# Performance work log

Measured on AMD Instinct MI355X. Metric: run time of the kernel, lower is better.

The kernel has to match this reference:

```python
import jax, jax.numpy as jnp
import numpy as np

D_MODEL = 1024
NUM_HEADS = 16
HEAD_DIM = D_MODEL // NUM_HEADS


def setup_inputs() -> dict:
    key = jax.random.key(0)
    ks = jax.random.split(key, 10)
    B, L = 2, 2048
    s = 1.0 / np.sqrt(D_MODEL)
    x = jax.random.normal(ks[0], (B, L, D_MODEL), dtype=jnp.float32)
    Wq = jax.random.normal(ks[1], (D_MODEL, D_MODEL), dtype=jnp.float32) * s
    bq = jnp.zeros((D_MODEL,), dtype=jnp.float32)
    Wk = jax.random.normal(ks[2], (D_MODEL, D_MODEL), dtype=jnp.float32) * s
    bk = jnp.zeros((D_MODEL,), dtype=jnp.float32)
    Wv = jax.random.normal(ks[3], (D_MODEL, D_MODEL), dtype=jnp.float32) * s
    bv = jnp.zeros((D_MODEL,), dtype=jnp.float32)
    Wo = jax.random.normal(ks[4], (D_MODEL, D_MODEL), dtype=jnp.float32) * s
    bo = jnp.zeros((D_MODEL,), dtype=jnp.float32)
    # per-head retention decay; torch init is ones, use values near 1 for nontrivial decay
    gamma = jax.random.uniform(ks[5], (NUM_HEADS,), dtype=jnp.float32, minval=0.95, maxval=1.0)
    return {"x": x, "Wq": Wq, "bq": bq, "Wk": Wk, "bk": bk,
            "Wv": Wv, "bv": bv, "Wo": Wo, "bo": bo, "gamma": gamma}


def reference(x, Wq, bq, Wk, bk, Wv, bv, Wo, bo, gamma):
    B, L, D = x.shape
    H, hd = NUM_HEADS, HEAD_DIM
    # projections (torch Linear: x @ W.T + b), split heads -> [B, H, L, hd]
    q = (x @ Wq.T + bq).reshape(B, L, H, hd).transpose(0, 2, 1, 3)
    k = (x @ Wk.T + bk).reshape(B, L, H, hd).transpose(0, 2, 1, 3)
    v = (x @ Wv.T + bv).reshape(B, L, H, hd).transpose(0, 2, 1, 3)
    # per-head decay gamma_h^i applied along the query index (matches torch broadcast)
    idx = jnp.arange(L, dtype=x.dtype)
    decay = gamma[None, :, None, None] ** idx[None, None, :, None]  # [1, H, L, 1]
    scores = jnp.einsum('bhqd,bhkd->bhqk', q, k)  # [B, H, L, L]
    causal = jnp.tril(jnp.ones((L, L), dtype=x.dtype))
    scores = scores * causal[None, None] * decay
    out = jnp.einsum('bhqk,bhkd->bhqd', scores, v)  # [B, H, L, hd]
    out = out.transpose(0, 2, 1, 3).reshape(B, L, D)
    return out @ Wo.T + bo
```

## Files before the change

### kernel.cpp

```cpp
#include <hip/hip_runtime.h>
#include <hip/hip_bf16.h>

#define D_MODEL 1024
#define NUM_HEADS 16
#define HEAD_DIM 64
#define BATCH 2
#define SEQ 2048
#define M_TOT (BATCH*SEQ)
#define CHUNK 64
#define NCHUNK (SEQ/CHUNK)
#define LT 68

typedef __attribute__((ext_vector_type(8))) short bf16x8;
typedef __attribute__((ext_vector_type(8))) unsigned short us16x8;
typedef __attribute__((ext_vector_type(4))) float f32x4;

__device__ inline ushort f2bf(float f) {
    __hip_bfloat16 h = __float2bfloat16(f);
    return __builtin_bit_cast(ushort, h);
}
__device__ inline float bf2f(ushort u) {
    unsigned int v = ((unsigned int)u) << 16;
    return __builtin_bit_cast(float, v);
}

__device__ inline bf16x8 ld_frag(const ushort* p) {
    struct S { uint2 a, b; };
    S s;
    s.a = *(const uint2*)p;
    s.b = *(const uint2*)(p + 4);
    return __builtin_bit_cast(bf16x8, s);
}

__device__ inline void st16(ushort* dst, uint4 a, uint4 b) {
    *(uint2*)(dst + 0)  = make_uint2(a.x, a.y);
    *(uint2*)(dst + 4)  = make_uint2(a.z, a.w);
    *(uint2*)(dst + 8)  = make_uint2(b.x, b.y);
    *(uint2*)(dst + 12) = make_uint2(b.z, b.w);
}

__device__ inline void load_lds16(const ushort* g, ushort* l) {
    __builtin_amdgcn_global_load_lds(
        (const __attribute__((address_space(1))) unsigned int*)g,
        (__attribute__((address_space(3))) unsigned int*)l, 16, 0, 0);
}

#define XN (M_TOT * D_MODEL)
#define WN (D_MODEL * D_MODEL)
#define CAST_BLOCKS ((XN + 4 * WN) / 4 / 256)
__global__ __launch_bounds__(256) void cast_all_kernel(const float* __restrict__ x,
                                                       const float* __restrict__ Wq,
                                                       const float* __restrict__ Wk,
                                                       const float* __restrict__ Wv,
                                                       const float* __restrict__ Wo,
                                                       ushort* __restrict__ dst,
                                                       const float* __restrict__ gamma,
                                                       float* __restrict__ decay) {
    int bx = blockIdx.x;
    if (bx >= CAST_BLOCKS) {
        int idx = (bx - CAST_BLOCKS) * 256 + threadIdx.x;
        int i = idx >> 4, h = idx & 15;
        decay[idx] = powf(gamma[h], (float)i);
        return;
    }
    size_t o = ((size_t)bx * 256 + threadIdx.x) * 4;
    const float* src;
    if (o < XN)               src = x  + o;
    else if (o < XN + WN)     src = Wq + (o - XN);
    else if (o < XN + 2 * WN) src = Wk + (o - XN - WN);
    else if (o < XN + 3 * WN) src = Wv + (o - XN - 2 * (size_t)WN);
    else                      src = Wo + (o - XN - 3 * (size_t)WN);
    float4 f = *(const float4*)src;
    ushort4 u;
    u.x = f2bf(f.x); u.y = f2bf(f.y); u.z = f2bf(f.z); u.w = f2bf(f.w);
    *(ushort4*)(dst + o) = u;
}

__global__ __launch_bounds__(256, 8) void gemm_qkv(const ushort* __restrict__ A,
                                                   const ushort* __restrict__ Bt,
                                                   const float* __restrict__ b0,
                                                   const float* __restrict__ b1,
                                                   const float* __restrict__ b2,
                                                   ushort* __restrict__ o0,
                                                   ushort* __restrict__ o1,
                                                   ushort* __restrict__ o2,
                                                   const float* __restrict__ decay) {
    const int K = 1024;
    __shared__ ushort lds_a[64 * 64];
    __shared__ ushort lds_b[64 * 64];
    int t = threadIdx.x, lane = t & 63, w = t >> 6;
    int bm = blockIdx.y * 64, bn = blockIdx.x * 64;
    int wm = (w >> 1) * 32, wn = (w & 1) * 32;

    int lr = lane >> 3, lc = lane & 7;
    int gcol = lc ^ (lr & 7);
    const ushort* aBase = A  + (size_t)(bm + w * 16 + lr) * K + gcol * 8;
    const ushort* bBase = Bt + (size_t)(bn + w * 16 + lr) * K + gcol * 8;
    ushort* aLds = &lds_a[(w * 16) * 64];
    ushort* bLds = &lds_b[(w * 16) * 64];

    f32x4 acc[2][2];
    #pragma unroll
    for (int i = 0; i < 2; i++)
        #pragma unroll
        for (int j = 0; j < 2; j++)
            acc[i][j] = (f32x4){0.f, 0.f, 0.f, 0.f};

    int mrel = lane & 15, kq = lane >> 4;

    for (int k0 = 0; k0 < K; k0 += 64) {
        load_lds16(aBase + k0, aLds);
        load_lds16(aBase + (size_t)8 * K + k0, aLds + 512);
        load_lds16(bBase + k0, bLds);
        load_lds16(bBase + (size_t)8 * K + k0, bLds + 512);
        __syncthreads();
        #pragma unroll
        for (int s = 0; s < 2; s++) {
            bf16x8 af[2], bfv[2];
            #pragma unroll
            for (int i = 0; i < 2; i++) {
                int row = wm + i * 16 + mrel;
                af[i] = ld_frag(&lds_a[row * 64 + (((s * 4 + kq) ^ (row & 7)) * 8)]);
            }
            #pragma unroll
            for (int j = 0; j < 2; j++) {
                int row = wn + j * 16 + mrel;
                bfv[j] = ld_frag(&lds_b[row * 64 + (((s * 4 + kq) ^ (row & 7)) * 8)]);
            }
            #pragma unroll
            for (int i = 0; i < 2; i++)
                #pragma unroll
                for (int j = 0; j < 2; j++)
                    acc[i][j] = __builtin_amdgcn_mfma_f32_16x16x32_bf16(af[i], bfv[j], acc[i][j], 0, 0, 0);
        }
        __syncthreads();
    }

    int quad = lane >> 4;
    int buf = bn >> 10;
    const float* bias = (buf == 0) ? b0 : (buf == 1) ? b1 : b2;
    ushort* dstv = (buf == 0) ? o0 : (buf == 1) ? o1 : o2;
    int cbase = (bn & 1023) + wn;
    #pragma unroll
    for (int j = 0; j < 2; j++) {
        int cl = cbase + j * 16 + mrel;
        float bv = bias[cl];
        #pragma unroll
        for (int i = 0; i < 2; i++) {
            #pragma unroll
            for (int reg = 0; reg < 4; reg++) {
                int row = bm + wm + i * 16 + quad * 4 + reg;
                float v = acc[i][j][reg] + bv;
                if (buf == 0)
                    v *= decay[(row & (SEQ - 1)) * 16 + (cl >> 6)];
                dstv[(size_t)row * 1024 + cl] = f2bf(v);
            }
        }
    }
}

__global__ __launch_bounds__(256) void gemm64_wo(const ushort* __restrict__ A,
                                                 const ushort* __restrict__ Bt,
                                                 const float* __restrict__ bias,
                                                 float* __restrict__ C) {
    const int K = 1024;
    __shared__ ushort lds_a[64 * 128];
    __shared__ ushort lds_b[64 * 128];
    int t = threadIdx.x, lane = t & 63, w = t >> 6;
    int bm = blockIdx.y * 64, bn = blockIdx.x * 64;
    int wm = (w >> 1) * 32, wn = (w & 1) * 32;

    int lr4 = lane >> 4;
    int lc16 = lane & 15;
    const ushort* aP[4];
    const ushort* bP[4];
    ushort* aL[4];
    ushort* bL[4];
    #pragma unroll
    for (int s = 0; s < 4; s++) {
        int rowRel = s * 4 + lr4;
        int gc = lc16 ^ (rowRel & 7);
        aP[s] = A  + (size_t)(bm + w * 16 + rowRel) * K + gc * 8;
        bP[s] = Bt + (size_t)(bn + w * 16 + rowRel) * K + gc * 8;
        aL[s] = &lds_a[(w * 16 + s * 4) * 128];
        bL[s] = &lds_b[(w * 16 + s * 4) * 128];
    }

    f32x4 acc[2][2];
    #pragma unroll
    for (int i = 0; i < 2; i++)
        #pragma unroll
        for (int j = 0; j < 2; j++)
            acc[i][j] = (f32x4){0.f, 0.f, 0.f, 0.f};

    int mrel = lane & 15, kq = lane >> 4;

    for (int k0 = 0; k0 < K; k0 += 128) {
        #pragma unroll
        for (int s = 0; s < 4; s++) {
            load_lds16(aP[s] + k0, aL[s]);
            load_lds16(bP[s] + k0, bL[s]);
        }
        __syncthreads();
        #pragma unroll
        for (int s = 0; s < 4; s++) {
            bf16x8 af[2], bfv[2];
            #pragma unroll
            for (int i = 0; i < 2; i++) {
                int row = wm + i * 16 + mrel;
                af[i] = ld_frag(&lds_a[row * 128 + (((s * 4 + kq) ^ (row & 7)) * 8)]);
            }
            #pragma unroll
            for (int j = 0; j < 2; j++) {
                int row = wn + j * 16 + mrel;
                bfv[j] = ld_frag(&lds_b[row * 128 + (((s * 4 + kq) ^ (row & 7)) * 8)]);
            }
            #pragma unroll
            for (int i = 0; i < 2; i++)
                #pragma unroll
                for (int j = 0; j < 2; j++)
                    acc[i][j] = __builtin_amdgcn_mfma_f32_16x16x32_bf16(af[i], bfv[j], acc[i][j], 0, 0, 0);
        }
        __syncthreads();
    }

    int quad = lane >> 4;
    #pragma unroll
    for (int j = 0; j < 2; j++) {
        int col = bn + wn + j * 16 + mrel;
        float bv = bias[col];
        #pragma unroll
        for (int i = 0; i < 2; i++) {
            #pragma unroll
            for (int reg = 0; reg < 4; reg++) {
                int row = bm + wm + i * 16 + quad * 4 + reg;
                C[(size_t)row * 1024 + col] = acc[i][j][reg] + bv;
            }
        }
    }
}

__global__ __launch_bounds__(256) void chunk_kv_mfma(const ushort* __restrict__ kp,
                                                     const ushort* __restrict__ vp,
                                                     ushort* __restrict__ statesb) {
    __shared__ ushort Kt[64 * LT];
    __shared__ ushort Vt[64 * LT];
    int bx = blockIdx.x;
    int c = bx & 31, h = (bx >> 5) & 15, b = bx >> 9;
    int t = threadIdx.x, lane = t & 63, w = t >> 6;
    size_t rowbase = (size_t)(b * SEQ + c * 64);
    int r = t >> 2, cc = t & 3;
    const uint4* gk = (const uint4*)(kp + (rowbase + r) * D_MODEL + h * 64 + cc * 16);
    const uint4* gv = (const uint4*)(vp + (rowbase + r) * D_MODEL + h * 64 + cc * 16);
    uint4 k0 = gk[0], k1 = gk[1], v0 = gv[0], v1 = gv[1];
    {
        us16x8 ka = __builtin_bit_cast(us16x8, k0), kb = __builtin_bit_cast(us16x8, k1);
        us16x8 va = __builtin_bit_cast(us16x8, v0), vb = __builtin_bit_cast(us16x8, v1);
        #pragma unroll
        for (int i = 0; i < 8; i++) {
            Kt[(cc * 16 + i) * LT + r]     = ka[i];
            Kt[(cc * 16 + 8 + i) * LT + r] = kb[i];
            Vt[(cc * 16 + i) * LT + r]     = va[i];
            Vt[(cc * 16 + 8 + i) * LT + r] = vb[i];
        }
    }
    __syncthreads();
    int mrel = lane & 15, q8 = (lane >> 4) * 8, band = w * 16, quad = lane >> 4;
    bf16x8 af[2];
    af[0] = ld_frag(&Vt[(band + mrel) * LT + q8]);
    af[1] = ld_frag(&Vt[(band + mrel) * LT + 32 + q8]);
    f32x4 acc[4];
    #pragma unroll
    for (int dt = 0; dt < 4; dt++) acc[dt] = (f32x4){0.f, 0.f, 0.f, 0.f};
    #pragma unroll
    for (int dt = 0; dt < 4; dt++)
        #pragma unroll
        for (int kk = 0; kk < 2; kk++)
            acc[dt] = __builtin_amdgcn_mfma_f32_16x16x32_bf16(
                af[kk], ld_frag(&Kt[(dt * 16 + mrel) * LT + kk * 32 + q8]), acc[dt], 0, 0, 0);
    __syncthreads();
    #pragma unroll
    for (int dt = 0; dt < 4; dt++)
        #pragma unroll
        for (int reg = 0; reg < 4; reg++)
            Kt[(band + quad * 4 + reg) * LT + dt * 16 + mrel] = f2bf(acc[dt][reg]);
    __syncthreads();
    {
        bf16x8 s0 = ld_frag(&Kt[r * LT + cc * 16]);
        bf16x8 s1 = ld_frag(&Kt[r * LT + cc * 16 + 8]);
        uint4* dst = (uint4*)(statesb + (size_t)bx * 4096 + r * 64 + cc * 16);
        dst[0] = __builtin_bit_cast(uint4, s0);
        dst[1] = __builtin_bit_cast(uint4, s1);
    }
}

__global__ __launch_bounds__(256) void prefix_kernel(ushort* __restrict__ statesb) {
    int bh = blockIdx.y;
    int e = blockIdx.x * 256 + threadIdx.x;
    ushort* p = statesb + (size_t)bh * NCHUNK * 4096 + e;
    float run = 0.f;
    for (int cb = 0; cb < NCHUNK; cb += 8) {
        float vals[8];
        #pragma unroll
        for (int u = 0; u < 8; u++) vals[u] = bf2f(p[(size_t)(cb + u) * 4096]);
        #pragma unroll
        for (int u = 0; u < 8; u++) {
            p[(size_t)(cb + u) * 4096] = f2bf(run);
            run += vals[u];
        }
    }
}

__global__ __launch_bounds__(256) void attn_mfma(const ushort* __restrict__ qp,
                                                 const ushort* __restrict__ kp,
                                                 const ushort* __restrict__ vp,
                                                 const ushort* __restrict__ statesb,
                                                 ushort* __restrict__ attn_out) {
    __shared__ ushort Qs[64 * LT];
    __shared__ ushort Ks[64 * LT];
    __shared__ ushort Vt[64 * LT];
    __shared__ ushort St[64 * LT];
    __shared__ ushort Ps[64 * LT];
    int bx = blockIdx.x;
    int c = bx & 31, h = (bx >> 5) & 15, b = bx >> 9;
    int t = threadIdx.x, lane = t & 63, w = t >> 6;
    size_t rowbase = (size_t)(b * SEQ + c * 64);
    int r = t >> 2, cc = t & 3;
    {
        const uint4* gq = (const uint4*)(qp + (rowbase + r) * D_MODEL + h * 64 + cc * 16);
        const uint4* gk = (const uint4*)(kp + (rowbase + r) * D_MODEL + h * 64 + cc * 16);
        const uint4* gv = (const uint4*)(vp + (rowbase + r) * D_MODEL + h * 64 + cc * 16);
        const uint4* gs = (const uint4*)(statesb + (size_t)bx * 4096 + t * 16);
        uint4 q0 = gq[0], q1 = gq[1];
        uint4 k0 = gk[0], k1 = gk[1];
        uint4 v0 = gv[0], v1 = gv[1];
        uint4 s0 = gs[0], s1 = gs[1];
        st16(&Qs[r * LT + cc * 16], q0, q1);
        st16(&Ks[r * LT + cc * 16], k0, k1);
        st16(&St[r * LT + cc * 16], s0, s1);
        us16x8 va = __builtin_bit_cast(us16x8, v0), vb = __builtin_bit_cast(us16x8, v1);
        #pragma unroll
        for (int i = 0; i < 8; i++) {
            Vt[(cc * 16 + i) * LT + r]     = va[i];
            Vt[(cc * 16 + 8 + i) * LT + r] = vb[i];
        }
    }
    __syncthreads();

    int mrel = lane & 15, q8 = (lane >> 4) * 8, quad = lane >> 4, band = w * 16;
    bf16x8 af[2];
    af[0] = ld_frag(&Qs[(band + mrel) * LT + q8]);
    af[1] = ld_frag(&Qs[(band + mrel) * LT + 32 + q8]);

    f32x4 oacc[4];
    #pragma unroll
    for (int dt = 0; dt < 4; dt++) oacc[dt] = (f32x4){0.f, 0.f, 0.f, 0.f};
    #pragma unroll
    for (int dt = 0; dt < 4; dt++)
        #pragma unroll
        for (int kk = 0; kk < 2; kk++)
            oacc[dt] = __builtin_amdgcn_mfma_f32_16x16x32_bf16(
                af[kk], ld_frag(&St[(dt * 16 + mrel) * LT + kk * 32 + q8]), oacc[dt], 0, 0, 0);

    f32x4 pacc[4];
    #pragma unroll
    for (int jt = 0; jt < 4; jt++) pacc[jt] = (f32x4){0.f, 0.f, 0.f, 0.f};
    #pragma unroll
    for (int jt = 0; jt < 4; jt++) {
        if (jt <= w) {
            #pragma unroll
            for (int kk = 0; kk < 2; kk++)
                pacc[jt] = __builtin_amdgcn_mfma_f32_16x16x32_bf16(
                    af[kk], ld_frag(&Ks[(jt * 16 + mrel) * LT + kk * 32 + q8]), pacc[jt], 0, 0, 0);
        }
    }
    #pragma unroll
    for (int jt = 0; jt < 4; jt++) {
        #pragma unroll
        for (int reg = 0; reg < 4; reg++) {
            int i = band + quad * 4 + reg;
            int j = jt * 16 + mrel;
            float val = (jt <= w && j <= i) ? pacc[jt][reg] : 0.f;
            Ps[i * LT + j] = f2bf(val);
        }
    }
    __syncthreads();

    bf16x8 pf0 = ld_frag(&Ps[(band + mrel) * LT + q8]);
    #pragma unroll
    for (int dt = 0; dt < 4; dt++)
        oacc[dt] = __builtin_amdgcn_mfma_f32_16x16x32_bf16(
            pf0, ld_frag(&Vt[(dt * 16 + mrel) * LT + q8]), oacc[dt], 0, 0, 0);
    if (w >= 2) {
        bf16x8 pf1 = ld_frag(&Ps[(band + mrel) * LT + 32 + q8]);
        #pragma unroll
        for (int dt = 0; dt < 4; dt++)
            oacc[dt] = __builtin_amdgcn_mfma_f32_16x16x32_bf16(
                pf1, ld_frag(&Vt[(dt * 16 + mrel) * LT + 32 + q8]), oacc[dt], 0, 0, 0);
    }

    #pragma unroll
    for (int dt = 0; dt < 4; dt++) {
        #pragma unroll
        for (int reg = 0; reg < 4; reg++) {
            size_t row = rowbase + band + quad * 4 + reg;
            int col = h * 64 + dt * 16 + mrel;
            attn_out[row * D_MODEL + col] = f2bf(oacc[dt][reg]);
        }
    }
}

extern "C" void kernel_launch(void* const* d_in, const int* in_sizes, int n_in,
                              void* d_out, int out_size, void* d_ws, size_t ws_size,
                              hipStream_t stream) {
    (void)in_sizes; (void)n_in; (void)out_size; (void)ws_size;
    const float* x  = (const float*)d_in[0];
    const float* Wq = (const float*)d_in[1];
    const float* bq = (const float*)d_in[2];
    const float* Wk = (const float*)d_in[3];
    const float* bk = (const float*)d_in[4];
    const float* Wv = (const float*)d_in[5];
    const float* bv = (const float*)d_in[6];
    const float* Wo = (const float*)d_in[7];
    const float* bo = (const float*)d_in[8];
    const float* gamma = (const float*)d_in[9];
    float* out = (float*)d_out;

    uint8_t* w = (uint8_t*)d_ws;
    ushort* xb    = (ushort*)w; w += (size_t)XN * 2;
    ushort* wqkvb = (ushort*)w; w += (size_t)3 * WN * 2;
    ushort* wob   = (ushort*)w; w += (size_t)WN * 2;
    ushort* qb  = (ushort*)w; w += (size_t)XN * 2;
    ushort* kb  = (ushort*)w; w += (size_t)XN * 2;
    ushort* vb  = (ushort*)w; w += (size_t)XN * 2;
    ushort* statesb = (ushort*)w; w += (size_t)BATCH * NUM_HEADS * NCHUNK * 4096 * 2;
    float*  decay = (float*)w; w += (size_t)SEQ * NUM_HEADS * 4;

    cast_all_kernel<<<CAST_BLOCKS + (SEQ * NUM_HEADS) / 256, 256, 0, stream>>>(
        x, Wq, Wk, Wv, Wo, xb, gamma, decay);

    gemm_qkv<<<dim3(3072 / 64, M_TOT / 64), 256, 0, stream>>>(
        xb, wqkvb, bq, bk, bv, qb, kb, vb, decay);

    int nblk = BATCH * NUM_HEADS * NCHUNK;
    chunk_kv_mfma<<<nblk, 256, 0, stream>>>(kb, vb, statesb);
    prefix_kernel<<<dim3(16, 32), 256, 0, stream>>>(statesb);
    attn_mfma<<<nblk, 256, 0, stream>>>(qb, kb, vb, statesb, xb);

    gemm64_wo<<<dim3(1024 / 64, M_TOT / 64), 256, 0, stream>>>(xb, wob, bo, out);
}
```

Baseline: 171.2 us.

## Share one A tile across Q, K and V projections in a fused QKV GEMM block

Each block now computes the matching 64x64 output tiles of Q, K and V together. One warp loads the A tile and the other three warps each load one weight tile, so every A tile is read once per k-step instead of three times. The grid shrinks from 48 to 16 column blocks, which leaves 1024 blocks in total. The cost is a larger LDS footprint (32KB), three times the accumulators per thread, a lower occupancy hint, and an uneven load split between the warps.

```diff
diff --git a/kernel.cpp b/kernel.cpp
--- a/kernel.cpp
+++ b/kernel.cpp
@@ -76,84 +76,89 @@
     *(ushort4*)(dst + o) = u;
 }
 
-__global__ __launch_bounds__(256, 8) void gemm_qkv(const ushort* __restrict__ A,
-                                                   const ushort* __restrict__ Bt,
-                                                   const float* __restrict__ b0,
-                                                   const float* __restrict__ b1,
-                                                   const float* __restrict__ b2,
-                                                   ushort* __restrict__ o0,
-                                                   ushort* __restrict__ o1,
-                                                   ushort* __restrict__ o2,
-                                                   const float* __restrict__ decay) {
+__global__ __launch_bounds__(256) void gemm_qkv(const ushort* __restrict__ A,
+                                                const ushort* __restrict__ Bt,
+                                                const float* __restrict__ b0,
+                                                const float* __restrict__ b1,
+                                                const float* __restrict__ b2,
+                                                ushort* __restrict__ o0,
+                                                ushort* __restrict__ o1,
+                                                ushort* __restrict__ o2,
+                                                const float* __restrict__ decay) {
     const int K = 1024;
-    __shared__ ushort lds_a[64 * 64];
-    __shared__ ushort lds_b[64 * 64];
+    __shared__ ushort lds[256 * 64];
     int t = threadIdx.x, lane = t & 63, w = t >> 6;
-    int bm = blockIdx.y * 64, bn = blockIdx.x * 64;
+    int bn = blockIdx.x * 64, bm = blockIdx.y * 64;
     int wm = (w >> 1) * 32, wn = (w & 1) * 32;
 
     int lr = lane >> 3, lc = lane & 7;
     int gcol = lc ^ (lr & 7);
-    const ushort* aBase = A  + (size_t)(bm + w * 16 + lr) * K + gcol * 8;
-    const ushort* bBase = Bt + (size_t)(bn + w * 16 + lr) * K + gcol * 8;
-    ushort* aLds = &lds_a[(w * 16) * 64];
-    ushort* bLds = &lds_b[(w * 16) * 64];
-
-    f32x4 acc[2][2];
-    #pragma unroll
-    for (int i = 0; i < 2; i++)
-        #pragma unroll
-        for (int j = 0; j < 2; j++)
-            acc[i][j] = (f32x4){0.f, 0.f, 0.f, 0.f};
+    const ushort* gbase = (w == 0)
+        ? (A  + (size_t)(bm + lr) * K + gcol * 8)
+        : (Bt + (size_t)((w - 1) * 1024 + bn + lr) * K + gcol * 8);
+    ushort* lbase = &lds[w * 64 * 64];
+
+    f32x4 acc[3][2][2];
+    #pragma unroll
+    for (int b = 0; b < 3; b++)
+        #pragma unroll
+        for (int i = 0; i < 2; i++)
+            #pragma unroll
+            for (int j = 0; j < 2; j++)
+                acc[b][i][j] = (f32x4){0.f, 0.f, 0.f, 0.f};
 
     int mrel = lane & 15, kq = lane >> 4;
 
     for (int k0 = 0; k0 < K; k0 += 64) {
-        load_lds16(aBase + k0, aLds);
-        load_lds16(aBase + (size_t)8 * K + k0, aLds + 512);
-        load_lds16(bBase + k0, bLds);
-        load_lds16(bBase + (size_t)8 * K + k0, bLds + 512);
+        #pragma unroll
+        for (int q = 0; q < 8; q++)
+            load_lds16(gbase + (size_t)q * 8 * K + k0, lbase + q * 512);
         __syncthreads();
         #pragma unroll
         for (int s = 0; s < 2; s++) {
-            bf16x8 af[2], bfv[2];
+            bf16x8 af[2];
             #pragma unroll
             for (int i = 0; i < 2; i++) {
                 int row = wm + i * 16 + mrel;
-                af[i] = ld_frag(&lds_a[row * 64 + (((s * 4 + kq) ^ (row & 7)) * 8)]);
-            }
-            #pragma unroll
-            for (int j = 0; j < 2; j++) {
-                int row = wn + j * 16 + mrel;
-                bfv[j] = ld_frag(&lds_b[row * 64 + (((s * 4 + kq) ^ (row & 7)) * 8)]);
-            }
-            #pragma unroll
-            for (int i = 0; i < 2; i++)
+                af[i] = ld_frag(&lds[row * 64 + (((s * 4 + kq) ^ (row & 7)) * 8)]);
+            }
+            #pragma unroll
+            for (int b = 0; b < 3; b++) {
+                bf16x8 bfv[2];
                 #pragma unroll
-                for (int j = 0; j < 2; j++)
-                    acc[i][j] = __builtin_amdgcn_mfma_f32_16x16x32_bf16(af[i], bfv[j], acc[i][j], 0, 0, 0);
+                for (int j = 0; j < 2; j++) {
+                    int rowb = wn + j * 16 + mrel;
+                    bfv[j] = ld_frag(&lds[(64 + b * 64 + rowb) * 64 + (((s * 4 + kq) ^ (rowb & 7)) * 8)]);
+                }
+                #pragma unroll
+                for (int i = 0; i < 2; i++)
+                    #pragma unroll
+                    for (int j = 0; j < 2; j++)
+                        acc[b][i][j] = __builtin_amdgcn_mfma_f32_16x16x32_bf16(af[i], bfv[j], acc[b][i][j], 0, 0, 0);
+            }
         }
         __syncthreads();
     }
 
     int quad = lane >> 4;
-    int buf = bn >> 10;
-    const float* bias = (buf == 0) ? b0 : (buf == 1) ? b1 : b2;
-    ushort* dstv = (buf == 0) ? o0 : (buf == 1) ? o1 : o2;
-    int cbase = (bn & 1023) + wn;
-    #pragma unroll
-    for (int j = 0; j < 2; j++) {
-        int cl = cbase + j * 16 + mrel;
-        float bv = bias[cl];
-        #pragma unroll
-        for (int i = 0; i < 2; i++) {
-            #pragma unroll
-            for (int reg = 0; reg < 4; reg++) {
-                int row = bm + wm + i * 16 + quad * 4 + reg;
-                float v = acc[i][j][reg] + bv;
-                if (buf == 0)
-                    v *= decay[(row & (SEQ - 1)) * 16 + (cl >> 6)];
-                dstv[(size_t)row * 1024 + cl] = f2bf(v);
+    #pragma unroll
+    for (int b = 0; b < 3; b++) {
+        const float* bias = (b == 0) ? b0 : (b == 1) ? b1 : b2;
+        ushort* dstv = (b == 0) ? o0 : (b == 1) ? o1 : o2;
+        #pragma unroll
+        for (int j = 0; j < 2; j++) {
+            int cl = bn + wn + j * 16 + mrel;
+            float bv = bias[cl];
+            #pragma unroll
+            for (int i = 0; i < 2; i++) {
+                #pragma unroll
+                for (int reg = 0; reg < 4; reg++) {
+                    int row = bm + wm + i * 16 + quad * 4 + reg;
+                    float v = acc[b][i][j][reg] + bv;
+                    if (b == 0)
+                        v *= decay[(row & (SEQ - 1)) * 16 + (cl >> 6)];
+                    dstv[(size_t)row * 1024 + cl] = f2bf(v);
+                }
             }
         }
     }
@@ -439,7 +444,7 @@
     cast_all_kernel<<<CAST_BLOCKS + (SEQ * NUM_HEADS) / 256, 256, 0, stream>>>(
         x, Wq, Wk, Wv, Wo, xb, gamma, decay);
 
-    gemm_qkv<<<dim3(3072 / 64, M_TOT / 64), 256, 0, stream>>>(
+    gemm_qkv<<<dim3(16, M_TOT / 64), 256, 0, stream>>>(
         xb, wqkvb, bq, bk, bv, qb, kb, vb, decay);
 
     int nblk = BATCH * NUM_HEADS * NCHUNK;
```

Result: no change. 170.2 us (-0.6%).
